# Kernel optimization log

Measured on AMD Instinct MI355X. Metric: run time of the kernel, lower is better.

## Reference

```python
import jax, jax.numpy as jnp
import numpy as np
import math

B, T, D = 2, 2048, 1024
H, HD = 16, 64
MAX_LEN = 2048


def _build_rope_sin_cos(max_seq, head_dim):
    inv_freq = 1.0 / 10000 ** (jnp.arange(0, head_dim, 2) / head_dim)
    positions = jnp.arange(max_seq)
    sinusoid_inp = jnp.einsum('i,j->ij', positions.astype(jnp.float32), inv_freq.astype(jnp.float32))
    sin = jnp.repeat(jnp.sin(sinusoid_inp), 2, axis=-1)
    cos = jnp.repeat(jnp.cos(sinusoid_inp), 2, axis=-1)
    return sin, cos


def _rotate_half(x):
    x1 = x[..., ::2]
    x2 = x[..., 1::2]
    return jnp.stack((-x2, x1), axis=-1).reshape(x.shape)


def setup_inputs() -> dict:
    key = jax.random.key(0)
    ks = jax.random.split(key, 6)
    x = jax.random.normal(ks[0], (B, T, D), dtype=jnp.float32)
    # causal boolean mask (B, T, T)
    mask = jnp.broadcast_to(jnp.tril(jnp.ones((T, T), dtype=bool)), (B, T, T))
    s = 1.0 / math.sqrt(D)
    wq = jax.random.normal(ks[1], (D, H, HD), dtype=jnp.float32) * s
    wk = jax.random.normal(ks[2], (D, H, HD), dtype=jnp.float32) * s
    wv = jax.random.normal(ks[3], (D, H, HD), dtype=jnp.float32) * s
    wo = jax.random.normal(ks[4], (H * HD, D), dtype=jnp.float32) * (1.0 / math.sqrt(H * HD))
    return {"x": x, "mask": mask, "wq": wq, "wk": wk, "wv": wv, "wo": wo}


def reference(x, mask, wq, wk, wv, wo):
    Bx, Tx, Dx = x.shape
    # q/k/v projections: DenseGeneral D -> (H, HD)
    q = jnp.einsum('btd,dhe->bthe', x, wq)
    k = jnp.einsum('btd,dhe->bthe', x, wk)
    v = jnp.einsum('btd,dhe->bthe', x, wv)
    sin, cos = _build_rope_sin_cos(MAX_LEN, HD)
    sin_t = sin[:Tx][None, :, None, :]
    cos_t = cos[:Tx][None, :, None, :]
    q = q * cos_t + _rotate_half(q) * sin_t
    k = k * cos_t + _rotate_half(k) * sin_t
    q = jnp.transpose(q, (0, 2, 1, 3))  # (B,H,T,HD)
    k = jnp.transpose(k, (0, 2, 1, 3))
    v = jnp.transpose(v, (0, 2, 1, 3))
    scale = 1.0 / math.sqrt(HD)
    logits = jnp.einsum('bhqd,bhkd->bhqk', q, k) * scale
    mask_f = mask[:, None, :, :].astype(jnp.float32)
    logits = logits + (1.0 - mask_f) * -1e10
    w = jax.nn.softmax(logits, axis=-1)
    attn_out = jnp.einsum('bhqk,bhkd->bhqd', w, v)
    attn_out = jnp.transpose(attn_out, (0, 2, 1, 3)).reshape(Bx, Tx, -1)
    return attn_out @ wo
```

## Files before the change

### kernel.cpp

```cpp
#include <hip/hip_runtime.h>
#include <cstdint>
#include <cstddef>

typedef __bf16 bf16x8 __attribute__((ext_vector_type(8)));
typedef __bf16 bf16x2 __attribute__((ext_vector_type(2)));
typedef float f32x4 __attribute__((ext_vector_type(4)));
typedef float f32x16 __attribute__((ext_vector_type(16)));
typedef unsigned int u32x4 __attribute__((ext_vector_type(4)));
#define UNROLL _Pragma("unroll")

__device__ __forceinline__ unsigned short f2bf(float f) {
  unsigned int x = __builtin_bit_cast(unsigned int, f);
  x += 0x7fffu + ((x >> 16) & 1u);
  return (unsigned short)(x >> 16);
}
__device__ __forceinline__ float bf2f(unsigned short u) {
  return __builtin_bit_cast(float, (unsigned int)u << 16);
}
__device__ __forceinline__ unsigned int cvtpk(float a, float b) {
  bf16x2 t; t[0] = (__bf16)a; t[1] = (__bf16)b;
  return __builtin_bit_cast(unsigned int, t);
}
__device__ __forceinline__ void async16(const void* g, void* l) {
  __builtin_amdgcn_global_load_lds((void __attribute__((address_space(1)))*)g,
                                   (void __attribute__((address_space(3)))*)l,
                                   16, 0, 0);
}

__global__ void prep_all(const float* __restrict__ x,
                         const float* __restrict__ wq, const float* __restrict__ wk,
                         const float* __restrict__ wv, const float* __restrict__ wo,
                         unsigned short* __restrict__ xb,
                         unsigned short* __restrict__ wT,
                         float2* __restrict__ ropetab) {
  __shared__ float tile[32][33];
  const int bx = blockIdx.x, tid = threadIdx.x;
  if (bx < 2048) {
    int i = bx * 256 + tid;
    const float4* p = (const float4*)(x + (size_t)i * 8);
    float4 a = p[0], b = p[1];
    ushort4 o0 = {f2bf(a.x), f2bf(a.y), f2bf(a.z), f2bf(a.w)};
    ushort4 o1 = {f2bf(b.x), f2bf(b.y), f2bf(b.z), f2bf(b.w)};
    ushort4* q = (ushort4*)(xb + (size_t)i * 8);
    q[0] = o0; q[1] = o1;
  } else if (bx < 6144) {
    const int idx = bx - 2048;
    const int z = idx >> 10;
    const float* src = z == 0 ? wq : z == 1 ? wk : z == 2 ? wv : wo;
    unsigned short* dst = wT + (size_t)z * 1048576;
    const int kb = (idx & 31) * 32, nb = ((idx >> 5) & 31) * 32;
    const int c = tid & 31, r4 = (tid >> 5) * 4;
UNROLL
    for (int i = 0; i < 4; ++i)
      tile[r4 + i][c] = src[(size_t)(kb + r4 + i) * 1024 + nb + c];
    __syncthreads();
UNROLL
    for (int i = 0; i < 4; ++i)
      dst[(size_t)(nb + r4 + i) * 1024 + kb + c] = f2bf(tile[c][r4 + i]);
  } else {
    int idx = (bx - 6144) * 256 + tid;
    int t = idx >> 5, i = idx & 31;
    float inv = exp2f(-(float)i * (13.287712379549449f / 32.0f));
    float ang = (float)t * inv;
    ropetab[idx] = make_float2(cosf(ang), sinf(ang));
  }
}

__global__ __launch_bounds__(256, 3) void gemmqkv(
    const unsigned short* __restrict__ A, const unsigned short* __restrict__ Bt,
    unsigned short* __restrict__ qout, unsigned short* __restrict__ kout,
    unsigned short* __restrict__ vtout, const float2* __restrict__ rope) {
  __shared__ __align__(16) unsigned short As[128 * 64];
  __shared__ __align__(16) unsigned short Bs[128 * 64];
  const int tid = threadIdx.x;
  const int lane = tid & 63, wid = tid >> 6;
  const int wr = wid >> 1, wc = wid & 1;
  const int g = lane >> 4, r16 = lane & 15;
  const int m0 = blockIdx.y * 128, n0 = blockIdx.x * 128;

  f32x4 acc[4][4];
UNROLL
  for (int i = 0; i < 4; ++i)
UNROLL
    for (int j = 0; j < 4; ++j) acc[i][j] = (f32x4){0.f, 0.f, 0.f, 0.f};

  const int ce = (((tid & 7) ^ ((tid >> 3) & 7)) << 3);
  const unsigned short* gA = A + (size_t)(m0 + (tid >> 3)) * 1024 + ce;
  const unsigned short* gB = Bt + (size_t)(n0 + (tid >> 3)) * 1024 + ce;
  char* lA = (char*)As + tid * 16;
  char* lB = (char*)Bs + tid * 16;

  const int swz = (r16 & 7) << 4;

  for (int u = 0; u < 16; ++u) {
    const int k0 = u * 64;
UNROLL
    for (int s = 0; s < 4; ++s) {
      async16(gA + (size_t)s * 32 * 1024 + k0, lA + s * 4096);
      async16(gB + (size_t)s * 32 * 1024 + k0, lB + s * 4096);
    }
    __syncthreads();
UNROLL
    for (int kk = 0; kk < 2; ++kk) {
      bf16x8 af[4], bfr[4];
UNROLL
      for (int mi = 0; mi < 4; ++mi)
        af[mi] = *(const bf16x8*)((const char*)As +
                  (wr * 64 + mi * 16 + r16) * 128 + ((kk * 64 + g * 16) ^ swz));
UNROLL
      for (int ni = 0; ni < 4; ++ni)
        bfr[ni] = *(const bf16x8*)((const char*)Bs +
                  (wc * 64 + ni * 16 + r16) * 128 + ((kk * 64 + g * 16) ^ swz));
UNROLL
      for (int mi = 0; mi < 4; ++mi)
UNROLL
        for (int ni = 0; ni < 4; ++ni)
          acc[mi][ni] = __builtin_amdgcn_mfma_f32_16x16x32_bf16(af[mi], bfr[ni],
                                                                acc[mi][ni], 0, 0, 0);
    }
    __syncthreads();
  }

  const int which = n0 >> 10;
  const int b = (m0 >= 2048) ? 1 : 0;
  const float QSCL = 0.18033688011112042f;
UNROLL
  for (int mi = 0; mi < 4; ++mi) {
    const int rowb = m0 + wr * 64 + mi * 16 + g * 4;
    const int trow = rowb & 2047;
UNROLL
    for (int ni = 0; ni < 4; ++ni) {
      const int n = n0 + wc * 64 + ni * 16 + r16;
      const int h = (n >> 6) & 15, e = n & 63;
      f32x4 v = acc[mi][ni];
      if (which < 2) {
        const int fi = e >> 1;
        const bool ev = (e & 1) == 0;
UNROLL
        for (int j = 0; j < 4; ++j) {
          float2 cs = rope[(trow + j) * 32 + fi];
          float p = __shfl_xor(v[j], 1);
          v[j] = ev ? (v[j] * cs.x - p * cs.y) : (v[j] * cs.x + p * cs.y);
        }
        if (which == 0) { v[0] *= QSCL; v[1] *= QSCL; v[2] *= QSCL; v[3] *= QSCL; }
      }
      if (which == 2) {
        size_t base = (((size_t)b * 16 + h) * 64 + e) * 2048 + trow;
        ushort4 pkv = {f2bf(v[0]), f2bf(v[1]), f2bf(v[2]), f2bf(v[3])};
        *(ushort4*)(vtout + base) = pkv;
      } else {
        unsigned short* dst = (which == 0) ? qout : kout;
        size_t base = (((size_t)b * 16 + h) * 2048 + trow) * 64 + e;
UNROLL
        for (int j = 0; j < 4; ++j) dst[base + (size_t)j * 64] = f2bf(v[j]);
      }
    }
  }
}

__global__ __launch_bounds__(256, 4) void gemm_o(
    const unsigned short* __restrict__ A, const unsigned short* __restrict__ Bt,
    float* __restrict__ out) {
  __shared__ __align__(16) unsigned short As[2][64 * 64];
  __shared__ __align__(16) unsigned short Bs[2][64 * 64];
  const int tid = threadIdx.x;
  const int lane = tid & 63, wid = tid >> 6;
  const int wm = wid >> 1, wn = wid & 1;
  const int g = lane >> 4, r16 = lane & 15;
  const int m0 = blockIdx.y * 64, n0 = blockIdx.x * 64;

  f32x4 acc[2][2];
UNROLL
  for (int i = 0; i < 2; ++i)
UNROLL
    for (int j = 0; j < 2; ++j) acc[i][j] = (f32x4){0.f, 0.f, 0.f, 0.f};

  const int ce = (((tid & 7) ^ ((tid >> 3) & 7)) << 3);
  const unsigned short* gA = A + (size_t)(m0 + (tid >> 3)) * 1024 + ce;
  const unsigned short* gB = Bt + (size_t)(n0 + (tid >> 3)) * 1024 + ce;
  const int dst0 = tid * 16;
  const int swz = (r16 & 7) << 4;

#define OSTG(bb, koff) { \
    async16(gA + (koff),             (char*)As[bb] + dst0); \
    async16(gA + 32 * 1024 + (koff), (char*)As[bb] + dst0 + 4096); \
    async16(gB + (koff),             (char*)Bs[bb] + dst0); \
    async16(gB + 32 * 1024 + (koff), (char*)Bs[bb] + dst0 + 4096); }

  OSTG(0, 0)
  for (int u = 0; u < 16; ++u) {
    const int bsel = u & 1;
    if (u + 1 < 16) { OSTG(bsel ^ 1, (u + 1) * 64) }
    __builtin_amdgcn_sched_barrier(0);
    if (u + 1 < 16) { asm volatile("s_waitcnt vmcnt(4)" ::: "memory"); }
    else            { asm volatile("s_waitcnt vmcnt(0)" ::: "memory"); }
    __builtin_amdgcn_s_barrier();
    __builtin_amdgcn_sched_barrier(0);
UNROLL
    for (int kk = 0; kk < 2; ++kk) {
      bf16x8 af[2], bfr[2];
UNROLL
      for (int mi = 0; mi < 2; ++mi)
        af[mi] = *(const bf16x8*)((const char*)As[bsel] +
                  (wm * 32 + mi * 16 + r16) * 128 + ((kk * 64 + g * 16) ^ swz));
UNROLL
      for (int ni = 0; ni < 2; ++ni)
        bfr[ni] = *(const bf16x8*)((const char*)Bs[bsel] +
                  (wn * 32 + ni * 16 + r16) * 128 + ((kk * 64 + g * 16) ^ swz));
UNROLL
      for (int mi = 0; mi < 2; ++mi)
UNROLL
        for (int ni = 0; ni < 2; ++ni)
          acc[mi][ni] = __builtin_amdgcn_mfma_f32_16x16x32_bf16(af[mi], bfr[ni],
                                                                acc[mi][ni], 0, 0, 0);
    }
    __builtin_amdgcn_sched_barrier(0);
    __builtin_amdgcn_s_barrier();
  }
#undef OSTG

UNROLL
  for (int mi = 0; mi < 2; ++mi) {
    const int rowb = m0 + wm * 32 + mi * 16 + g * 4;
UNROLL
    for (int ni = 0; ni < 2; ++ni) {
      const int n = n0 + wn * 32 + ni * 16 + r16;
UNROLL
      for (int j = 0; j < 4; ++j)
        out[(size_t)(rowb + j) * 1024 + n] = acc[mi][ni][j];
    }
  }
}

__device__ const signed char c_qt[32]   = {15,15,10,10,15,14,14,14,13, 9, 9, 4,13,13,12,12, 8, 8,12,11,11,11, 7, 7, 3, 6, 6, 5, 5, 2, 1, 0};
__device__ const signed char c_t0[32]   = { 0,11, 0,11,22, 0,10,20, 0, 0,10, 0,10,19, 0, 9, 0, 9,18, 0, 8,16, 0, 8, 0, 0, 7, 0, 6, 0, 0, 0};
__device__ const signed char c_len[32]  = {11,11,11,11,10,10,10,10,10,10,10,10, 9, 9, 9, 9, 9, 9, 8, 8, 8, 8, 8, 8, 8, 7, 7, 6, 6, 6, 4, 2};
__device__ const signed char c_slot[32] = {24,25,10,11,26,21,22,23,18, 8, 9,-1,19,20,15,16, 6, 7,17,12,13,14, 4, 5,-1, 2, 3, 0, 1,-1,-1,-1};

__global__ __launch_bounds__(256, 2) void attn4(
    const unsigned short* __restrict__ qb, const unsigned short* __restrict__ kb,
    const unsigned short* __restrict__ vtb, unsigned short* __restrict__ attnb,
    unsigned short* __restrict__ po, float* __restrict__ ml) {
  __shared__ __align__(16) char smem[4][16384];
  const int tid = threadIdx.x;
  const int lane = tid & 63, w = tid >> 6;
  const int l31 = lane & 31, h = lane >> 5;
  const int bh = blockIdx.x;
  const int item = blockIdx.y;
  const int qt = c_qt[item];
  const int t0 = c_t0[item];
  const int t1 = t0 + c_len[item];
  const int slot = c_slot[item];
  const int q0w = qt * 128 + w * 32;
  const int qg = q0w + l31;
  const size_t kvbase = (size_t)bh * (2048 * 64);

  bf16x8 qf[4];
  const unsigned short* qp = qb + kvbase + (size_t)qg * 64 + h * 8;
UNROLL
  for (int kk = 0; kk < 4; ++kk) qf[kk] = *(const bf16x8*)(qp + kk * 16);

  u32x4 of; of[0] = of[1] = of[2] = of[3] = 0x3F803F80u;
  const bf16x8 onesf = __builtin_bit_cast(bf16x8, of);

  const int lr = lane >> 3;
  const int cb2 = ((lane & 7) ^ lr) << 3;
  const bool isK = (w < 2);
  const int c0 = isK ? w * 4 : (w - 2) * 4;
  const unsigned short* srcp[4];
  int dstoff[4];
  const size_t step = isK ? 4096 : 64;
UNROLL
  for (int s = 0; s < 4; ++s) {
    int r = (c0 + s) * 8 + lr;
    srcp[s] = isK ? (kb + kvbase + (size_t)r * 64 + cb2)
                  : (vtb + kvbase + (size_t)r * 2048 + cb2);
    dstoff[s] = (w * 4 + s) * 1024 + lane * 16;
  }

  f32x16 o0, o1, lacc;
UNROLL
  for (int r = 0; r < 16; ++r) { o0[r] = 0.f; o1[r] = 0.f; lacc[r] = 0.f; }

#define STAGE_T(tv, bufv) { \
    const int tc_ = ((tv) < t1) ? (tv) : (t1 - 1); \
    char* db_ = &smem[(bufv)][0]; \
    async16(srcp[0] + (size_t)tc_ * step, db_ + dstoff[0]); \
    async16(srcp[1] + (size_t)tc_ * step, db_ + dstoff[1]); \
    async16(srcp[2] + (size_t)tc_ * step, db_ + dstoff[2]); \
    async16(srcp[3] + (size_t)tc_ * step, db_ + dstoff[3]); }

  const int np = (t1 - t0 + 1) >> 1;
  STAGE_T(t0, 0) STAGE_T(t0 + 1, 1)
  if (np > 1) { STAGE_T(t0 + 2, 2) STAGE_T(t0 + 3, 3) }

  const int swz = (l31 & 7) << 4;
  for (int p = 0; p < np; ++p) {
    const int tp = t0 + 2 * p;
    __builtin_amdgcn_sched_barrier(0);
    if (p + 1 < np) { asm volatile("s_waitcnt vmcnt(8)" ::: "memory"); }
    else            { asm volatile("s_waitcnt vmcnt(0)" ::: "memory"); }
    __builtin_amdgcn_s_barrier();
    __builtin_amdgcn_sched_barrier(0);
UNROLL
    for (int sub = 0; sub < 2; ++sub) {
      const int t = tp + sub;
      const int kt0 = t << 6;
      if (t < t1 && kt0 <= q0w + 31) {
        const char* cbuf = &smem[(2 * p + sub) & 3][0];
        f32x16 sa, sb;
UNROLL
        for (int r = 0; r < 16; ++r) { sa[r] = 0.f; sb[r] = 0.f; }
        __builtin_amdgcn_s_setprio(1);
UNROLL
        for (int kk = 0; kk < 4; ++kk) {
          bf16x8 kf = *(const bf16x8*)(cbuf + l31 * 128 + ((kk * 32 + h * 16) ^ swz));
          sa = __builtin_amdgcn_mfma_f32_32x32x16_bf16(kf, qf[kk], sa, 0, 0, 0);
        }
UNROLL
        for (int kk = 0; kk < 4; ++kk) {
          bf16x8 kf = *(const bf16x8*)(cbuf + (32 + l31) * 128 + ((kk * 32 + h * 16) ^ swz));
          sb = __builtin_amdgcn_mfma_f32_32x32x16_bf16(kf, qf[kk], sb, 0, 0, 0);
        }
        __builtin_amdgcn_s_setprio(0);
        if (kt0 + 63 > q0w) {
UNROLL
          for (int r = 0; r < 16; ++r) {
            int koff = (r & 3) + 8 * (r >> 2) + 4 * h;
            if (kt0 + koff > qg) sa[r] = -3e38f;
            if (kt0 + 32 + koff > qg) sb[r] = -3e38f;
          }
        }
UNROLL
        for (int r = 0; r < 16; ++r) {
          sa[r] = exp2f(sa[r]);
          sb[r] = exp2f(sb[r]);
        }
        unsigned int lo[8], hi[8];
UNROLL
        for (int b8 = 0; b8 < 4; ++b8) {
          lo[b8]     = cvtpk(sa[4 * b8], sa[4 * b8 + 1]);
          hi[b8]     = cvtpk(sa[4 * b8 + 2], sa[4 * b8 + 3]);
          lo[4 + b8] = cvtpk(sb[4 * b8], sb[4 * b8 + 1]);
          hi[4 + b8] = cvtpk(sb[4 * b8 + 2], sb[4 * b8 + 3]);
        }
        bf16x8 pa[4];
UNROLL
        for (int j = 0; j < 4; ++j) {
          const int bb = (j >> 1) * 4 + (j & 1) * 2;
          unsigned int a0 = lo[bb], b0 = lo[bb + 1];
          unsigned int a1 = hi[bb], b1 = hi[bb + 1];
          asm volatile("v_permlane32_swap_b32 %0, %1" : "+v"(a0), "+v"(b0));
          asm volatile("v_permlane32_swap_b32 %0, %1" : "+v"(a1), "+v"(b1));
          u32x4 f;
          f[0] = a0; f[1] = a1; f[2] = b0; f[3] = b1;
          pa[j] = __builtin_bit_cast(bf16x8, f);
        }
        __builtin_amdgcn_s_setprio(1);
UNROLL
        for (int j = 0; j < 4; ++j) {
          bf16x8 v0 = *(const bf16x8*)(cbuf + 8192 + l31 * 128 + ((j * 32 + h * 16) ^ swz));
          bf16x8 v1 = *(const bf16x8*)(cbuf + 8192 + (32 + l31) * 128 + ((j * 32 + h * 16) ^ swz));
          o0 = __builtin_amdgcn_mfma_f32_32x32x16_bf16(pa[j], v0, o0, 0, 0, 0);
          o1 = __builtin_amdgcn_mfma_f32_32x32x16_bf16(pa[j], v1, o1, 0, 0, 0);
          lacc = __builtin_amdgcn_mfma_f32_32x32x16_bf16(pa[j], onesf, lacc, 0, 0, 0);
        }
        __builtin_amdgcn_s_setprio(0);
      }
    }
    __builtin_amdgcn_sched_barrier(0);
    __builtin_amdgcn_s_barrier();
    if (p + 2 < np) { STAGE_T(tp + 4, (2 * p) & 3) STAGE_T(tp + 5, (2 * p + 1) & 3) }
  }
#undef STAGE_T

  if (slot < 0) {
    const int b = bh >> 4, hh = bh & 15;
UNROLL
    for (int r = 0; r < 16; ++r) {
      const int qg2 = q0w + (r & 3) + 8 * (r >> 2) + 4 * h;
      const size_t base = (((size_t)b * 2048 + qg2) * 16 + hh) * 64 + l31;
      const float iv = 1.0f / lacc[r];
      attnb[base]      = f2bf(o0[r] * iv);
      attnb[base + 32] = f2bf(o1[r] * iv);
    }
  } else {
    const int p = bh * 27 + slot;
    if (l31 == 0) {
UNROLL
      for (int r = 0; r < 16; ++r)
        ml[p * 128 + w * 32 + (r & 3) + 8 * (r >> 2) + 4 * h] = lacc[r];
    }
    unsigned short* pb = po + (size_t)p * 8192;
UNROLL
    for (int r = 0; r < 16; ++r) {
      const int rl = w * 32 + (r & 3) + 8 * (r >> 2) + 4 * h;
      const float iv = 1.0f / lacc[r];
      pb[rl * 64 + l31]      = f2bf(o0[r] * iv);
      pb[rl * 64 + l31 + 32] = f2bf(o1[r] * iv);
    }
  }
}

__global__ void attn_combine(const unsigned short* __restrict__ po,
                             const float* __restrict__ ml,
                             unsigned short* __restrict__ attnb) {
  const int idx = blockIdx.x * 256 + threadIdx.x;
  const int cg = idx & 3;
  const int row = (idx >> 2) & 127;
  const int t2 = idx >> 9;
  const int qi = t2 % 11;
  const int bh = t2 / 11;
  const int qt = qi + 5;
  const int cnt = (qt < 11) ? 2 : 3;
  const int base = (qt < 11) ? (qt - 5) * 2 : 12 + (qt - 11) * 3;
  const int slotg = bh * 27 + base;
  float acc[16];
UNROLL
  for (int i = 0; i < 16; ++i) acc[i] = 0.f;
  float wsum = 0.f;
  for (int i = 0; i < cnt; ++i) {
    const float l = ml[(slotg + i) * 128 + row];
    wsum += l;
    const ushort4* p = (const ushort4*)(po + (size_t)(slotg + i) * 8192 + row * 64 + cg * 16);
UNROLL
    for (int v = 0; v < 4; ++v) {
      ushort4 u = p[v];
      acc[v * 4 + 0] += l * bf2f(u.x);
      acc[v * 4 + 1] += l * bf2f(u.y);
      acc[v * 4 + 2] += l * bf2f(u.z);
      acc[v * 4 + 3] += l * bf2f(u.w);
    }
  }
  const float inv = 1.0f / wsum;
  const int b = bh >> 4, hh = bh & 15;
  const int q = qt * 128 + row;
  ushort4* out = (ushort4*)(attnb + (((size_t)b * 2048 + q) * 16 + hh) * 64 + cg * 16);
UNROLL
  for (int v = 0; v < 4; ++v) {
    ushort4 o;
    o.x = f2bf(acc[v * 4 + 0] * inv);
    o.y = f2bf(acc[v * 4 + 1] * inv);
    o.z = f2bf(acc[v * 4 + 2] * inv);
    o.w = f2bf(acc[v * 4 + 3] * inv);
    out[v] = o;
  }
}

extern "C" void kernel_launch(void* const* d_in, const int* in_sizes, int n_in,
                              void* d_out, int out_size, void* d_ws, size_t ws_size,
                              hipStream_t stream) {
  (void)in_sizes; (void)n_in; (void)out_size; (void)ws_size;
  const float* x = (const float*)d_in[0];
  const float* wq = (const float*)d_in[2];
  const float* wk = (const float*)d_in[3];
  const float* wv = (const float*)d_in[4];
  const float* wo = (const float*)d_in[5];

  unsigned short* xb = (unsigned short*)d_ws;
  unsigned short* wT = xb + 4 * 1024 * 1024;
  float2* rope = (float2*)(wT + 4 * 1024 * 1024);
  unsigned short* qb = (unsigned short*)(rope + 65536);
  unsigned short* kbuf = qb + 4 * 1024 * 1024;
  unsigned short* vtb = kbuf + 4 * 1024 * 1024;
  unsigned short* attnb = vtb + 4 * 1024 * 1024;

  unsigned short* po = xb;
  float* mlb = (float*)rope;

  prep_all<<<dim3(6400), dim3(256), 0, stream>>>(x, wq, wk, wv, wo, xb, wT, rope);
  gemmqkv<<<dim3(24, 32), dim3(256), 0, stream>>>(xb, wT, qb, kbuf, vtb, rope);
  attn4<<<dim3(32, 32), dim3(256), 0, stream>>>(qb, kbuf, vtb, attnb, po, mlb);
  attn_combine<<<dim3(704), dim3(256), 0, stream>>>(po, mlb, attnb);
  gemm_o<<<dim3(16, 64), dim3(256), 0, stream>>>(attnb, wT + 3 * 1024 * 1024,
                                                 (float*)d_out);
}
```

Before: 107.6 us.

## Widen attention query tile to 256 rows with 512-thread blocks and double buffering

The attention kernel now gives each block 256 query rows with 8 waves, so every staged K/V tile is shared by twice as many query rows. Global loads are spread over 8 waves at 2 loads each. The 4-deep, two-tiles-per-step pipeline becomes a simpler double buffer, one tile per iteration. The causal work split tables and the partial-combine indexing are rebuilt for 15 work items per head, which changes load balance and reduces prefetch depth.

```diff
diff --git a/kernel.cpp b/kernel.cpp
--- a/kernel.cpp
+++ b/kernel.cpp
@@ -232,26 +232,26 @@
   }
 }
 
-__device__ const signed char c_qt[32]   = {15,15,10,10,15,14,14,14,13, 9, 9, 4,13,13,12,12, 8, 8,12,11,11,11, 7, 7, 3, 6, 6, 5, 5, 2, 1, 0};
-__device__ const signed char c_t0[32]   = { 0,11, 0,11,22, 0,10,20, 0, 0,10, 0,10,19, 0, 9, 0, 9,18, 0, 8,16, 0, 8, 0, 0, 7, 0, 6, 0, 0, 0};
-__device__ const signed char c_len[32]  = {11,11,11,11,10,10,10,10,10,10,10,10, 9, 9, 9, 9, 9, 9, 8, 8, 8, 8, 8, 8, 8, 7, 7, 6, 6, 6, 4, 2};
-__device__ const signed char c_slot[32] = {24,25,10,11,26,21,22,23,18, 8, 9,-1,19,20,15,16, 6, 7,17,12,13,14, 4, 5,-1, 2, 3, 0, 1,-1,-1,-1};
-
-__global__ __launch_bounds__(256, 2) void attn4(
+__device__ const signed char a_qt[15]   = { 6, 6, 5, 5, 7, 7, 7, 4, 4, 3, 3, 1, 2, 2, 0};
+__device__ const signed char a_t0[15]   = { 0,14, 0,12, 0,11,22, 0,10, 0, 8, 0, 0, 6, 0};
+__device__ const signed char a_len[15]  = {14,14,12,12,11,11,10,10,10, 8, 8, 8, 6, 6, 4};
+__device__ const signed char a_slot[15] = { 8, 9, 6, 7,10,11,12, 4, 5, 2, 3,-1, 0, 1,-1};
+
+__global__ __launch_bounds__(512, 4) void attn5(
     const unsigned short* __restrict__ qb, const unsigned short* __restrict__ kb,
     const unsigned short* __restrict__ vtb, unsigned short* __restrict__ attnb,
     unsigned short* __restrict__ po, float* __restrict__ ml) {
-  __shared__ __align__(16) char smem[4][16384];
+  __shared__ __align__(16) char smem[2][16384];
   const int tid = threadIdx.x;
   const int lane = tid & 63, w = tid >> 6;
   const int l31 = lane & 31, h = lane >> 5;
   const int bh = blockIdx.x;
   const int item = blockIdx.y;
-  const int qt = c_qt[item];
-  const int t0 = c_t0[item];
-  const int t1 = t0 + c_len[item];
-  const int slot = c_slot[item];
-  const int q0w = qt * 128 + w * 32;
+  const int qt = a_qt[item];
+  const int t0 = a_t0[item];
+  const int t1 = t0 + a_len[item];
+  const int slot = a_slot[item];
+  const int q0w = qt * 256 + w * 32;
   const int qg = q0w + l31;
   const size_t kvbase = (size_t)bh * (2048 * 64);
 
@@ -265,114 +265,105 @@
 
   const int lr = lane >> 3;
   const int cb2 = ((lane & 7) ^ lr) << 3;
-  const bool isK = (w < 2);
-  const int c0 = isK ? w * 4 : (w - 2) * 4;
-  const unsigned short* srcp[4];
-  int dstoff[4];
+  const bool isK = (w < 4);
+  const int wk4 = w & 3;
+  const unsigned short* srcp[2];
+  int dstoff[2];
   const size_t step = isK ? 4096 : 64;
 UNROLL
-  for (int s = 0; s < 4; ++s) {
-    int r = (c0 + s) * 8 + lr;
+  for (int s = 0; s < 2; ++s) {
+    const int r = (wk4 * 2 + s) * 8 + lr;
     srcp[s] = isK ? (kb + kvbase + (size_t)r * 64 + cb2)
                   : (vtb + kvbase + (size_t)r * 2048 + cb2);
-    dstoff[s] = (w * 4 + s) * 1024 + lane * 16;
+    dstoff[s] = (isK ? 0 : 8192) + (wk4 * 2 + s) * 1024 + lane * 16;
   }
 
   f32x16 o0, o1, lacc;
 UNROLL
   for (int r = 0; r < 16; ++r) { o0[r] = 0.f; o1[r] = 0.f; lacc[r] = 0.f; }
 
-#define STAGE_T(tv, bufv) { \
-    const int tc_ = ((tv) < t1) ? (tv) : (t1 - 1); \
-    char* db_ = &smem[(bufv)][0]; \
-    async16(srcp[0] + (size_t)tc_ * step, db_ + dstoff[0]); \
-    async16(srcp[1] + (size_t)tc_ * step, db_ + dstoff[1]); \
-    async16(srcp[2] + (size_t)tc_ * step, db_ + dstoff[2]); \
-    async16(srcp[3] + (size_t)tc_ * step, db_ + dstoff[3]); }
-
-  const int np = (t1 - t0 + 1) >> 1;
-  STAGE_T(t0, 0) STAGE_T(t0 + 1, 1)
-  if (np > 1) { STAGE_T(t0 + 2, 2) STAGE_T(t0 + 3, 3) }
+  async16(srcp[0] + (size_t)t0 * step, &smem[0][0] + dstoff[0]);
+  async16(srcp[1] + (size_t)t0 * step, &smem[0][0] + dstoff[1]);
 
   const int swz = (l31 & 7) << 4;
-  for (int p = 0; p < np; ++p) {
-    const int tp = t0 + 2 * p;
-    __builtin_amdgcn_sched_barrier(0);
-    if (p + 1 < np) { asm volatile("s_waitcnt vmcnt(8)" ::: "memory"); }
-    else            { asm volatile("s_waitcnt vmcnt(0)" ::: "memory"); }
+  for (int t = t0; t < t1; ++t) {
+    const int kt0 = t << 6;
+    if (t + 1 < t1) {
+      char* db = &smem[(t + 1 - t0) & 1][0];
+      async16(srcp[0] + (size_t)(t + 1) * step, db + dstoff[0]);
+      async16(srcp[1] + (size_t)(t + 1) * step, db + dstoff[1]);
+      __builtin_amdgcn_sched_barrier(0);
+      asm volatile("s_waitcnt vmcnt(2)" ::: "memory");
+    } else {
+      __builtin_amdgcn_sched_barrier(0);
+      asm volatile("s_waitcnt vmcnt(0)" ::: "memory");
+    }
     __builtin_amdgcn_s_barrier();
     __builtin_amdgcn_sched_barrier(0);
-UNROLL
-    for (int sub = 0; sub < 2; ++sub) {
-      const int t = tp + sub;
-      const int kt0 = t << 6;
-      if (t < t1 && kt0 <= q0w + 31) {
-        const char* cbuf = &smem[(2 * p + sub) & 3][0];
-        f32x16 sa, sb;
-UNROLL
-        for (int r = 0; r < 16; ++r) { sa[r] = 0.f; sb[r] = 0.f; }
-        __builtin_amdgcn_s_setprio(1);
-UNROLL
-        for (int kk = 0; kk < 4; ++kk) {
-          bf16x8 kf = *(const bf16x8*)(cbuf + l31 * 128 + ((kk * 32 + h * 16) ^ swz));
-          sa = __builtin_amdgcn_mfma_f32_32x32x16_bf16(kf, qf[kk], sa, 0, 0, 0);
+    if (kt0 <= q0w + 31) {
+      const char* cbuf = &smem[(t - t0) & 1][0];
+      f32x16 sa, sb;
+UNROLL
+      for (int r = 0; r < 16; ++r) { sa[r] = 0.f; sb[r] = 0.f; }
+      __builtin_amdgcn_s_setprio(1);
+UNROLL
+      for (int kk = 0; kk < 4; ++kk) {
+        bf16x8 kf = *(const bf16x8*)(cbuf + l31 * 128 + ((kk * 32 + h * 16) ^ swz));
+        sa = __builtin_amdgcn_mfma_f32_32x32x16_bf16(kf, qf[kk], sa, 0, 0, 0);
+      }
+UNROLL
+      for (int kk = 0; kk < 4; ++kk) {
+        bf16x8 kf = *(const bf16x8*)(cbuf + (32 + l31) * 128 + ((kk * 32 + h * 16) ^ swz));
+        sb = __builtin_amdgcn_mfma_f32_32x32x16_bf16(kf, qf[kk], sb, 0, 0, 0);
+      }
+      __builtin_amdgcn_s_setprio(0);
+      if (kt0 + 63 > q0w) {
+UNROLL
+        for (int r = 0; r < 16; ++r) {
+          int koff = (r & 3) + 8 * (r >> 2) + 4 * h;
+          if (kt0 + koff > qg) sa[r] = -3e38f;
+          if (kt0 + 32 + koff > qg) sb[r] = -3e38f;
         }
-UNROLL
-        for (int kk = 0; kk < 4; ++kk) {
-          bf16x8 kf = *(const bf16x8*)(cbuf + (32 + l31) * 128 + ((kk * 32 + h * 16) ^ swz));
-          sb = __builtin_amdgcn_mfma_f32_32x32x16_bf16(kf, qf[kk], sb, 0, 0, 0);
-        }
-        __builtin_amdgcn_s_setprio(0);
-        if (kt0 + 63 > q0w) {
-UNROLL
-          for (int r = 0; r < 16; ++r) {
-            int koff = (r & 3) + 8 * (r >> 2) + 4 * h;
-            if (kt0 + koff > qg) sa[r] = -3e38f;
-            if (kt0 + 32 + koff > qg) sb[r] = -3e38f;
-          }
-        }
-UNROLL
-        for (int r = 0; r < 16; ++r) {
-          sa[r] = exp2f(sa[r]);
-          sb[r] = exp2f(sb[r]);
-        }
-        unsigned int lo[8], hi[8];
-UNROLL
-        for (int b8 = 0; b8 < 4; ++b8) {
-          lo[b8]     = cvtpk(sa[4 * b8], sa[4 * b8 + 1]);
-          hi[b8]     = cvtpk(sa[4 * b8 + 2], sa[4 * b8 + 3]);
-          lo[4 + b8] = cvtpk(sb[4 * b8], sb[4 * b8 + 1]);
-          hi[4 + b8] = cvtpk(sb[4 * b8 + 2], sb[4 * b8 + 3]);
-        }
-        bf16x8 pa[4];
-UNROLL
-        for (int j = 0; j < 4; ++j) {
-          const int bb = (j >> 1) * 4 + (j & 1) * 2;
-          unsigned int a0 = lo[bb], b0 = lo[bb + 1];
-          unsigned int a1 = hi[bb], b1 = hi[bb + 1];
-          asm volatile("v_permlane32_swap_b32 %0, %1" : "+v"(a0), "+v"(b0));
-          asm volatile("v_permlane32_swap_b32 %0, %1" : "+v"(a1), "+v"(b1));
-          u32x4 f;
-          f[0] = a0; f[1] = a1; f[2] = b0; f[3] = b1;
-          pa[j] = __builtin_bit_cast(bf16x8, f);
-        }
-        __builtin_amdgcn_s_setprio(1);
-UNROLL
-        for (int j = 0; j < 4; ++j) {
-          bf16x8 v0 = *(const bf16x8*)(cbuf + 8192 + l31 * 128 + ((j * 32 + h * 16) ^ swz));
-          bf16x8 v1 = *(const bf16x8*)(cbuf + 8192 + (32 + l31) * 128 + ((j * 32 + h * 16) ^ swz));
-          o0 = __builtin_amdgcn_mfma_f32_32x32x16_bf16(pa[j], v0, o0, 0, 0, 0);
-          o1 = __builtin_amdgcn_mfma_f32_32x32x16_bf16(pa[j], v1, o1, 0, 0, 0);
-          lacc = __builtin_amdgcn_mfma_f32_32x32x16_bf16(pa[j], onesf, lacc, 0, 0, 0);
-        }
-        __builtin_amdgcn_s_setprio(0);
-      }
+      }
+UNROLL
+      for (int r = 0; r < 16; ++r) {
+        sa[r] = exp2f(sa[r]);
+        sb[r] = exp2f(sb[r]);
+      }
+      unsigned int lo[8], hi[8];
+UNROLL
+      for (int b8 = 0; b8 < 4; ++b8) {
+        lo[b8]     = cvtpk(sa[4 * b8], sa[4 * b8 + 1]);
+        hi[b8]     = cvtpk(sa[4 * b8 + 2], sa[4 * b8 + 3]);
+        lo[4 + b8] = cvtpk(sb[4 * b8], sb[4 * b8 + 1]);
+        hi[4 + b8] = cvtpk(sb[4 * b8 + 2], sb[4 * b8 + 3]);
+      }
+      bf16x8 pa[4];
+UNROLL
+      for (int j = 0; j < 4; ++j) {
+        const int bb = (j >> 1) * 4 + (j & 1) * 2;
+        unsigned int a0 = lo[bb], b0 = lo[bb + 1];
+        unsigned int a1 = hi[bb], b1 = hi[bb + 1];
+        asm volatile("v_permlane32_swap_b32 %0, %1" : "+v"(a0), "+v"(b0));
+        asm volatile("v_permlane32_swap_b32 %0, %1" : "+v"(a1), "+v"(b1));
+        u32x4 f;
+        f[0] = a0; f[1] = a1; f[2] = b0; f[3] = b1;
+        pa[j] = __builtin_bit_cast(bf16x8, f);
+      }
+      __builtin_amdgcn_s_setprio(1);
+UNROLL
+      for (int j = 0; j < 4; ++j) {
+        bf16x8 v0 = *(const bf16x8*)(cbuf + 8192 + l31 * 128 + ((j * 32 + h * 16) ^ swz));
+        bf16x8 v1 = *(const bf16x8*)(cbuf + 8192 + (32 + l31) * 128 + ((j * 32 + h * 16) ^ swz));
+        o0 = __builtin_amdgcn_mfma_f32_32x32x16_bf16(pa[j], v0, o0, 0, 0, 0);
+        o1 = __builtin_amdgcn_mfma_f32_32x32x16_bf16(pa[j], v1, o1, 0, 0, 0);
+        lacc = __builtin_amdgcn_mfma_f32_32x32x16_bf16(pa[j], onesf, lacc, 0, 0, 0);
+      }
+      __builtin_amdgcn_s_setprio(0);
     }
     __builtin_amdgcn_sched_barrier(0);
     __builtin_amdgcn_s_barrier();
-    if (p + 2 < np) { STAGE_T(tp + 4, (2 * p) & 3) STAGE_T(tp + 5, (2 * p + 1) & 3) }
-  }
-#undef STAGE_T
+  }
 
   if (slot < 0) {
     const int b = bh >> 4, hh = bh & 15;
@@ -385,13 +376,13 @@
       attnb[base + 32] = f2bf(o1[r] * iv);
     }
   } else {
-    const int p = bh * 27 + slot;
+    const int p = bh * 13 + slot;
     if (l31 == 0) {
 UNROLL
       for (int r = 0; r < 16; ++r)
-        ml[p * 128 + w * 32 + (r & 3) + 8 * (r >> 2) + 4 * h] = lacc[r];
-    }
-    unsigned short* pb = po + (size_t)p * 8192;
+        ml[p * 256 + w * 32 + (r & 3) + 8 * (r >> 2) + 4 * h] = lacc[r];
+    }
+    unsigned short* pb = po + (size_t)p * 16384;
 UNROLL
     for (int r = 0; r < 16; ++r) {
       const int rl = w * 32 + (r & 3) + 8 * (r >> 2) + 4 * h;
@@ -407,22 +398,22 @@
                              unsigned short* __restrict__ attnb) {
   const int idx = blockIdx.x * 256 + threadIdx.x;
   const int cg = idx & 3;
-  const int row = (idx >> 2) & 127;
-  const int t2 = idx >> 9;
-  const int qi = t2 % 11;
-  const int bh = t2 / 11;
-  const int qt = qi + 5;
-  const int cnt = (qt < 11) ? 2 : 3;
-  const int base = (qt < 11) ? (qt - 5) * 2 : 12 + (qt - 11) * 3;
-  const int slotg = bh * 27 + base;
+  const int row = (idx >> 2) & 255;
+  const int t2 = idx >> 10;
+  const int qi = t2 % 6;
+  const int bh = t2 / 6;
+  const int qt = qi + 2;
+  const int cnt = (qt == 7) ? 3 : 2;
+  const int base = (qt < 7) ? (qt - 2) * 2 : 10;
+  const int slotg = bh * 13 + base;
   float acc[16];
 UNROLL
   for (int i = 0; i < 16; ++i) acc[i] = 0.f;
   float wsum = 0.f;
   for (int i = 0; i < cnt; ++i) {
-    const float l = ml[(slotg + i) * 128 + row];
+    const float l = ml[(slotg + i) * 256 + row];
     wsum += l;
-    const ushort4* p = (const ushort4*)(po + (size_t)(slotg + i) * 8192 + row * 64 + cg * 16);
+    const ushort4* p = (const ushort4*)(po + (size_t)(slotg + i) * 16384 + row * 64 + cg * 16);
 UNROLL
     for (int v = 0; v < 4; ++v) {
       ushort4 u = p[v];
@@ -434,7 +425,7 @@
   }
   const float inv = 1.0f / wsum;
   const int b = bh >> 4, hh = bh & 15;
-  const int q = qt * 128 + row;
+  const int q = qt * 256 + row;
   ushort4* out = (ushort4*)(attnb + (((size_t)b * 2048 + q) * 16 + hh) * 64 + cg * 16);
 UNROLL
   for (int v = 0; v < 4; ++v) {
@@ -470,8 +461,8 @@
 
   prep_all<<<dim3(6400), dim3(256), 0, stream>>>(x, wq, wk, wv, wo, xb, wT, rope);
   gemmqkv<<<dim3(24, 32), dim3(256), 0, stream>>>(xb, wT, qb, kbuf, vtb, rope);
-  attn4<<<dim3(32, 32), dim3(256), 0, stream>>>(qb, kbuf, vtb, attnb, po, mlb);
-  attn_combine<<<dim3(704), dim3(256), 0, stream>>>(po, mlb, attnb);
+  attn5<<<dim3(32, 15), dim3(512), 0, stream>>>(qb, kbuf, vtb, attnb, po, mlb);
+  attn_combine<<<dim3(768), dim3(256), 0, stream>>>(po, mlb, attnb);
   gemm_o<<<dim3(16, 64), dim3(256), 0, stream>>>(attnb, wT + 3 * 1024 * 1024,
                                                  (float*)d_out);
 }
```

Result: slower. 112.6 us (+4.6%).
